# Kernel tuning notes

Measured on AMD Instinct MI355X. Metric: run time of the kernel, lower is better.

The kernel has to match this reference:

```python
import jax, jax.numpy as jnp
import numpy as np

T_MIN, T_MAX = 0.6, 1.6
SIM_LO, SIM_HI = 0.5, 0.9
LN_EPS = 1e-5


def _layernorm(x, gamma, beta):
    mu = jnp.mean(x, axis=-1, keepdims=True)
    var = jnp.mean((x - mu) ** 2, axis=-1, keepdims=True)
    return (x - mu) * jax.lax.rsqrt(var + LN_EPS) * gamma + beta


def _cos_sim(a, b, eps=1e-8):
    num = jnp.sum(a * b, axis=-1)
    na = jnp.maximum(jnp.sqrt(jnp.sum(a * a, axis=-1)), eps)
    nb = jnp.maximum(jnp.sqrt(jnp.sum(b * b, axis=-1)), eps)
    return num / (na * nb)


def setup_inputs() -> dict:
    key = jax.random.key(0)
    B, L, D = 2, 4096, 512
    ks = jax.random.split(key, 10)
    s = 0.02
    return {
        "x": jax.random.normal(ks[0], (B, L, D), dtype=jnp.float32),
        "Wq": jax.random.normal(ks[1], (D, D), dtype=jnp.float32) * s,
        "Wk": jax.random.normal(ks[2], (D, D), dtype=jnp.float32) * s,
        "Wv": jax.random.normal(ks[3], (D, D), dtype=jnp.float32) * s,
        "Wp": jax.random.normal(ks[4], (D, D), dtype=jnp.float32) * s,
        "W1": jax.random.normal(ks[5], (4 * D, D), dtype=jnp.float32) * s,
        "b1": jnp.zeros((4 * D,), dtype=jnp.float32),
        "W2": jax.random.normal(ks[6], (D, 4 * D), dtype=jnp.float32) * s,
        "b2": jnp.zeros((D,), dtype=jnp.float32),
        "gamma": jnp.ones((D,), dtype=jnp.float32),
        "beta": jnp.zeros((D,), dtype=jnp.float32),
    }


def reference(x, Wq, Wk, Wv, Wp, W1, b1, W2, b2, gamma, beta):
    B, L, D = x.shape
    xn = _layernorm(x, gamma, beta)
    # TinyAttn with T=1.0, causal=True (torch Linear: x @ W.T)
    Q = jnp.einsum("bld,ed->ble", xn, Wq)
    K = jnp.einsum("bld,ed->ble", xn, Wk)
    V = jnp.einsum("bld,ed->ble", xn, Wv)
    scores = jnp.einsum("bld,bmd->blm", Q, K) / jnp.sqrt(jnp.asarray(D, x.dtype))
    causal = jnp.triu(jnp.ones((L, L), dtype=bool), 1)
    scores = jnp.where(causal, jnp.asarray(-1e30, x.dtype), scores)
    attn = jax.nn.softmax(scores, axis=-1)  # [B, L, L]
    out = jnp.einsum("blm,bmd->bld", attn, V)
    out = jnp.einsum("bld,ed->ble", out, Wp)
    ctx = x + out
    h = _layernorm(ctx, gamma, beta)
    h = jax.nn.gelu(jnp.einsum("bld,fd->blf", h, W1) + b1, approximate=False)
    ctx = ctx + jnp.einsum("blf,df->bld", h, W2) + b2

    # AdaptiveController on last-token attention row
    last_attn = attn[:, -1]  # [B, L]
    p = jnp.clip(last_attn, 1e-9, None)
    H = -jnp.sum(p * jnp.log(p), axis=-1)  # [B]
    Hn = (H - H.min()) / (H.max() - H.min() + 1e-9)
    Hm = jax.lax.stop_gradient(jnp.mean(Hn))  # detached in torch
    T = T_MIN + (T_MAX - T_MIN) * Hm
    sim_th = SIM_HI - (SIM_HI - SIM_LO) * Hm

    # UnconsciousStack: single forward -> stack holds only the just-pushed (K, V), detached.
    q_vec = jnp.mean(Q[:, -1], axis=0, keepdims=True)  # [1, D]
    K_rep = jax.lax.stop_gradient(jnp.mean(K, axis=1))  # [B, D]
    s = jnp.mean(_cos_sim(q_vec, K_rep))  # scalar
    hit = s >= sim_th

    K_cat = jnp.concatenate([K, jax.lax.stop_gradient(K)], axis=1)  # [B, 2L, D]
    V_cat = jnp.concatenate([V, jax.lax.stop_gradient(V)], axis=1)
    scores2 = jnp.einsum("bld,bmd->blm", Q, K_cat) / jnp.sqrt(jnp.asarray(D, x.dtype))
    attn2 = jax.nn.softmax(scores2 / T, axis=-1)  # [B, L, 2L], no causal mask
    reatt = jnp.einsum("blm,bmd->bld", attn2, V_cat)
    ctx = ctx + jnp.where(hit, reatt, jnp.zeros_like(reatt))
    return ctx
```

## Files before the change

kernel.cpp:

```cpp
#include <hip/hip_runtime.h>
#include <math.h>

#define BATCH 2
#define SEQ 4096
#define DIM 512
#define FF 2048
#define NROWS (BATCH*SEQ)
#define KT 32
#define RSQRT_D 0.044194173824159216f

typedef __attribute__((ext_vector_type(8))) short short8;
typedef __attribute__((ext_vector_type(4))) short short4v;
typedef __attribute__((ext_vector_type(4))) float f32x4;

__device__ __forceinline__ float gelu_f(float v) {
    return 0.5f * v * (1.0f + erff(v * 0.70710678118654752440f));
}
__device__ __forceinline__ short bf16b(float x) {
    union { float f; unsigned u; } c; c.f = x;
    unsigned r = (c.u + 0x7FFFu + ((c.u >> 16) & 1u)) >> 16;
    return (short)r;
}
__device__ __forceinline__ float bf16f(short h) {
    union { unsigned u; float f; } c; c.u = ((unsigned)(unsigned short)h) << 16;
    return c.f;
}
__device__ __forceinline__ void gload16(const void* g, void* l) {
    __builtin_amdgcn_global_load_lds(
        (const __attribute__((address_space(1))) unsigned int*)g,
        (__attribute__((address_space(3))) unsigned int*)l, 16, 0, 0);
}
__device__ __forceinline__ float blk_sum256(float v, volatile float* sm) {
    #pragma unroll
    for (int o = 32; o; o >>= 1) v += __shfl_xor(v, o);
    __syncthreads();
    if ((threadIdx.x & 63) == 0) sm[threadIdx.x >> 6] = v;
    __syncthreads();
    return sm[0] + sm[1] + sm[2] + sm[3];
}

__global__ __launch_bounds__(256) void f2bf_all(
        const float* __restrict__ Wq, const float* __restrict__ Wk,
        const float* __restrict__ Wv, const float* __restrict__ Wp,
        const float* __restrict__ W1, const float* __restrict__ W2,
        short* __restrict__ Wcat, short* __restrict__ Wpb,
        short* __restrict__ W1b, short* __restrict__ W2b)
{
    int i = blockIdx.x * 256 + threadIdx.x;
    const float* src; short* dst; int loc;
    if      (i <  32768) { src = Wq; dst = Wcat;          loc = i; }
    else if (i <  65536) { src = Wk; dst = Wcat + 262144; loc = i - 32768; }
    else if (i <  98304) { src = Wv; dst = Wcat + 524288; loc = i - 65536; }
    else if (i < 131072) { src = Wp; dst = Wpb;           loc = i - 98304; }
    else if (i < 262144) { src = W1; dst = W1b;           loc = i - 131072; }
    else                 { src = W2; dst = W2b;           loc = i - 262144; }
    const float4* p = (const float4*)(src + (size_t)loc * 8);
    float4 a = p[0], b = p[1];
    short8 r;
    r[0]=bf16b(a.x); r[1]=bf16b(a.y); r[2]=bf16b(a.z); r[3]=bf16b(a.w);
    r[4]=bf16b(b.x); r[5]=bf16b(b.y); r[6]=bf16b(b.z); r[7]=bf16b(b.w);
    *(short8*)(dst + (size_t)loc * 8) = r;
}

__global__ __launch_bounds__(256) void ln_kernel(const float* __restrict__ x,
        const float* __restrict__ g, const float* __restrict__ be,
        short* __restrict__ o)
{
    int row  = blockIdx.x * 4 + (threadIdx.x >> 6);
    int lane = threadIdx.x & 63;
    const float4* xr = (const float4*)(x + (size_t)row * DIM);
    float4 v0 = xr[lane*2], v1 = xr[lane*2+1];
    float s = v0.x+v0.y+v0.z+v0.w + v1.x+v1.y+v1.z+v1.w;
    #pragma unroll
    for (int off = 32; off; off >>= 1) s += __shfl_xor(s, off);
    float mu = s * (1.0f/DIM);
    float d[8] = {v0.x-mu, v0.y-mu, v0.z-mu, v0.w-mu, v1.x-mu, v1.y-mu, v1.z-mu, v1.w-mu};
    float q = 0.f;
    #pragma unroll
    for (int j = 0; j < 8; ++j) q += d[j]*d[j];
    #pragma unroll
    for (int off = 32; off; off >>= 1) q += __shfl_xor(q, off);
    float rs = rsqrtf(q * (1.0f/DIM) + 1e-5f);
    const float4* g4 = (const float4*)g;
    const float4* b4 = (const float4*)be;
    float4 ga = g4[lane*2], gb = g4[lane*2+1];
    float4 ba = b4[lane*2], bb = b4[lane*2+1];
    float gv[8] = {ga.x,ga.y,ga.z,ga.w, gb.x,gb.y,gb.z,gb.w};
    float bv[8] = {ba.x,ba.y,ba.z,ba.w, bb.x,bb.y,bb.z,bb.w};
    short8 r;
    #pragma unroll
    for (int j = 0; j < 8; ++j) r[j] = bf16b(d[j]*rs*gv[j] + bv[j]);
    *(short8*)(o + (size_t)row * DIM + lane*8) = r;
}

template<int TM, int TAG>
__global__ __launch_bounds__(256) void gemm_v3(
        const short* __restrict__ A, const short* __restrict__ W,
        const float* __restrict__ bias, const float* __restrict__ res,
        float* __restrict__ Cf, short* __restrict__ Cb,
        short* __restrict__ CbK, short* __restrict__ CbV,
        int K, int sa, int sw, int sc, int act, int accum)
{
    constexpr int MI = TM / 32;
    __shared__ short As[2][TM*32];
    __shared__ short Ws[2][4096];
    int tid = threadIdx.x;
    int m0 = blockIdx.y * TM, n0 = blockIdx.x * 128;
    int w = tid >> 6, lane = tid & 63;
    int wr = (w >> 1) * (TM/2), wc = (w & 1) * 64;
    int lr = lane & 15, lg = lane >> 4;
    int srow = tid >> 2, skoff = (tid & 3) * 8;
    const short* Ab = A + (size_t)(m0 + srow) * sa + skoff;
    const short* Wb = W + (size_t)(n0 + srow) * sw + skoff;

    #define STAGE_G(buf, kk) do { \
        gload16(Ab + (kk),                    As[buf] + tid*8); \
        if constexpr (TM == 128) \
            gload16(Ab + (size_t)64*sa + (kk), As[buf] + 2048 + tid*8); \
        gload16(Wb + (kk),                    Ws[buf] + tid*8); \
        gload16(Wb + (size_t)64*sw + (kk),    Ws[buf] + 2048 + tid*8); } while(0)

    f32x4 acc[MI][4];
    f32x4 zero = {0.f, 0.f, 0.f, 0.f};
    #pragma unroll
    for (int i = 0; i < MI; ++i)
        #pragma unroll
        for (int j = 0; j < 4; ++j) acc[i][j] = zero;

    STAGE_G(0, 0);
    __syncthreads();
    int cur = 0;
    for (int k0 = 0; k0 < K; k0 += 32) {
        if (k0 + 32 < K) STAGE_G(cur ^ 1, k0 + 32);
        short8 a[MI], b[4];
        #pragma unroll
        for (int i = 0; i < MI; ++i) a[i] = *(const short8*)(As[cur] + (wr + i*16 + lr)*32 + lg*8);
        #pragma unroll
        for (int j = 0; j < 4; ++j) b[j] = *(const short8*)(Ws[cur] + (wc + j*16 + lr)*32 + lg*8);
        #pragma unroll
        for (int i = 0; i < MI; ++i)
            #pragma unroll
            for (int j = 0; j < 4; ++j)
                acc[i][j] = __builtin_amdgcn_mfma_f32_16x16x32_bf16(a[i], b[j], acc[i][j], 0, 0, 0);
        __syncthreads();
        cur ^= 1;
    }
    #undef STAGE_G

    #pragma unroll
    for (int i = 0; i < MI; ++i) {
        #pragma unroll
        for (int r = 0; r < 4; ++r) {
            size_t m = (size_t)m0 + wr + i*16 + lg*4 + r;
            #pragma unroll
            for (int j = 0; j < 4; ++j) {
                int n = n0 + wc + j*16 + lr;
                float v = acc[i][j][r];
                if (bias) v += bias[n];
                if (act)  v = gelu_f(v);
                if (CbK) {
                    int seg = n >> 9, nl = n & 511;
                    short* dst = (seg == 0) ? Cb : (seg == 1) ? CbK : CbV;
                    dst[m * 512 + nl] = bf16b(v);
                } else {
                    if (res) v += res[m * sc + n];
                    size_t idx = m * sc + n;
                    if (Cf) { if (accum) Cf[idx] += v; else Cf[idx] = v; }
                    if (Cb) Cb[idx] = bf16b(v);
                }
            }
        }
    }
}

__global__ __launch_bounds__(256) void vtrans(const short* __restrict__ V,
                                              short* __restrict__ Vt)
{
    __shared__ short t_s[64][72];
    int l0 = blockIdx.x * 64, d0 = blockIdx.y * 64, b = blockIdx.z;
    int t = threadIdx.x;
    const short* src = V + (size_t)b * SEQ * DIM;
    #pragma unroll
    for (int it = 0; it < 2; ++it) {
        int r = (t >> 3) + it * 32, c = (t & 7) * 8;
        *(short8*)&t_s[r][c] = *(const short8*)(src + (size_t)(l0 + r) * DIM + d0 + c);
    }
    __syncthreads();
    short* dst = Vt + (size_t)b * DIM * SEQ;
    #pragma unroll
    for (int it = 0; it < 2; ++it) {
        int r = (t >> 3) + it * 32, c = (t & 7) * 8;
        short8 v;
        #pragma unroll
        for (int j = 0; j < 8; ++j) v[j] = t_s[c + j][r];
        *(short8*)(dst + (size_t)(d0 + r) * SEQ + l0 + c) = v;
    }
}

__global__ __launch_bounds__(512, 2) void attn_v8(
        const short* __restrict__ Q, const short* __restrict__ K,
        const short* __restrict__ Vt, short* __restrict__ Opart,
        float* __restrict__ Mpart, float* __restrict__ Lpart,
        float scale, const float* __restrict__ scale_ptr,
        const float* __restrict__ gate, int causal, int NC, int ncs)
{
    if (gate && gate[0] == 0.0f) return;
    if (scale_ptr) scale = scale_ptr[0];
    extern __shared__ short lds[];
    short* k_s  = lds;
    short* v_s  = lds + 32768;
    short* p_s  = lds + 65536;
    float* ss_s = (float*)(lds + 69632);

    int tid = threadIdx.x, w = tid >> 6, lane = tid & 63;
    int rg = w >> 1, dh = w & 1;
    int lr = lane & 15, lg = lane >> 4;

    int bid = blockIdx.x;
    int c  = bid & (NC - 1);
    int b  = (bid >> ncs) & 1;
    int ip = bid >> (ncs + 1);
    int jj0 = ip, jj1 = 63 - ip;
    int TA = causal ? 2*(ip+1)  : 128;
    int TB = causal ? 2*(64-ip) : 128;
    int Ttot = TA + TB;
    int s0 = (Ttot * c) >> ncs, s1 = (Ttot * (c+1)) >> ncs;

    size_t bofs = (size_t)b * SEQ * DIM;
    size_t vofs = (size_t)b * DIM * SEQ;
    f32x4 zero = {0.f, 0.f, 0.f, 0.f};

    for (int sg = 0; sg < 2; ++sg) {
        int j  = sg ? jj1 : jj0;
        int ta = sg ? (max(s0, TA) - TA) : s0;
        int tb = sg ? (s1 - TA)          : min(s1, TA);
        if (ta >= tb) continue;
        int qw0 = j*64 + rg*16;

        short8 qf[8];
        #pragma unroll
        for (int kc = 0; kc < 8; ++kc)
            qf[kc] = *(const short8*)(Q + bofs + (size_t)(qw0 + lr)*DIM
                                      + dh*256 + kc*32 + lg*8);

        f32x4 o[16];
        #pragma unroll
        for (int df = 0; df < 16; ++df) o[df] = zero;
        float mreg[4] = {-1e30f,-1e30f,-1e30f,-1e30f};
        float lreg[4] = {0.f,0.f,0.f,0.f};
        int rowg[4];
        #pragma unroll
        for (int r = 0; r < 4; ++r) rowg[r] = qw0 + lg*4 + r;

        int cur = 0;
        {
            int k0s = ta * KT;
            #pragma unroll
            for (int s4 = 0; s4 < 4; ++s4) {
                int slot = tid + s4*512;
                int row = slot >> 6, cg = slot & 63;
                gload16(K + bofs + (size_t)(k0s + row)*DIM + ((cg ^ (row & 7)) << 3),
                        k_s + slot*8);
                int dpair = slot >> 3, low = slot & 7;
                int d = dpair*2 + (low & 1);
                int kg = (low >> 1) ^ (dpair & 3);
                gload16(Vt + vofs + (size_t)d*SEQ + k0s + kg*8,
                        v_s + slot*8);
            }
        }
        __syncthreads();

        for (int t = ta; t < tb; ++t) {
            int k0 = t * KT;
            if (t + 1 < tb) {
                int k0s = (t + 1) * KT;
                int bo = (cur ^ 1) * 16384;
                #pragma unroll
                for (int s4 = 0; s4 < 4; ++s4) {
                    int slot = tid + s4*512;
                    int row = slot >> 6, cg = slot & 63;
                    gload16(K + bofs + (size_t)(k0s + row)*DIM + ((cg ^ (row & 7)) << 3),
                            k_s + bo + slot*8);
                    int dpair = slot >> 3, low = slot & 7;
                    int d = dpair*2 + (low & 1);
                    int kg = (low >> 1) ^ (dpair & 3);
                    gload16(Vt + vofs + (size_t)d*SEQ + k0s + kg*8,
                            v_s + bo + slot*8);
                }
            }
            f32x4 ss[2];
            ss[0] = zero; ss[1] = zero;
            const short* kb = k_s + cur*16384;
            #pragma unroll
            for (int kc = 0; kc < 8; ++kc) {
                #pragma unroll
                for (int kf = 0; kf < 2; ++kf) {
                    int row = kf*16 + lr;
                    int dg = dh*32 + kc*4 + lg;
                    short8 kk = *(const short8*)(kb + row*512 + ((dg ^ (row & 7)) << 3));
                    ss[kf] = __builtin_amdgcn_mfma_f32_16x16x32_bf16(qf[kc], kk, ss[kf], 0, 0, 0);
                }
            }
            *(f32x4*)(ss_s + w*512 + lane*8)     = ss[0];
            *(f32x4*)(ss_s + w*512 + lane*8 + 4) = ss[1];
            asm volatile("s_waitcnt lgkmcnt(0)" ::: "memory");
            __builtin_amdgcn_s_barrier();
            __builtin_amdgcn_sched_barrier(0);
            f32x4 po0 = *(const f32x4*)(ss_s + (w^1)*512 + lane*8);
            f32x4 po1 = *(const f32x4*)(ss_s + (w^1)*512 + lane*8 + 4);
            bool needmask = causal && (k0 + KT - 1 > qw0);
            #pragma unroll
            for (int r = 0; r < 4; ++r) {
                float s0v = (ss[0][r] + po0[r]) * scale;
                float s1v = (ss[1][r] + po1[r]) * scale;
                if (needmask) {
                    if (k0 + lr      > rowg[r]) s0v = -1e30f;
                    if (k0 + 16 + lr > rowg[r]) s1v = -1e30f;
                }
                ss[0][r] = s0v; ss[1][r] = s1v;
            }
            float pm[4];
            bool tg = false;
            #pragma unroll
            for (int r = 0; r < 4; ++r) {
                pm[r] = fmaxf(ss[0][r], ss[1][r]);
                tg |= (pm[r] > mreg[r] + 8.0f);
            }
            if (__any(tg)) {
                #pragma unroll
                for (int r = 0; r < 4; ++r) {
                    float v = pm[r];
                    v = fmaxf(v, __shfl_xor(v, 1));
                    v = fmaxf(v, __shfl_xor(v, 2));
                    v = fmaxf(v, __shfl_xor(v, 4));
                    v = fmaxf(v, __shfl_xor(v, 8));
                    float nm = fmaxf(mreg[r], v);
                    float fr = __expf(mreg[r] - nm);
                    mreg[r] = nm;
                    lreg[r] *= fr;
                    #pragma unroll
                    for (int df = 0; df < 16; ++df) o[df][r] *= fr;
                }
            }
            #pragma unroll
            for (int kf = 0; kf < 2; ++kf) {
                #pragma unroll
                for (int r = 0; r < 4; ++r) {
                    float sv = ss[kf][r];
                    float p = (sv < -1e29f) ? 0.0f : __expf(sv - mreg[r]);
                    lreg[r] += p;
                    int row = lg*4 + r;
                    int oct = kf*2 + (lr >> 3);
                    p_s[w*512 + row*32 + ((oct ^ r ^ (lg & 3)) << 3) + (lr & 7)] = bf16b(p);
                }
            }
            short8 pa = *(const short8*)(p_s + w*512 + lr*32
                         + ((lg ^ (lr & 3) ^ ((lr >> 2) & 3)) << 3));
            const short* vb = v_s + cur*16384;
            #pragma unroll
            for (int df = 0; df < 16; ++df) {
                int d = dh*256 + df*16 + lr;
                int slot16 = (d >> 1)*8 + (((lg ^ ((d >> 1) & 3)) << 1) | (d & 1));
                short8 vv = *(const short8*)(vb + slot16*8);
                o[df] = __builtin_amdgcn_mfma_f32_16x16x32_bf16(pa, vv, o[df], 0, 0, 0);
            }
            __syncthreads();
            cur ^= 1;
        }

        #pragma unroll
        for (int r = 0; r < 4; ++r) {
            float v = lreg[r];
            v += __shfl_xor(v, 1);
            v += __shfl_xor(v, 2);
            v += __shfl_xor(v, 4);
            v += __shfl_xor(v, 8);
            lreg[r] = v;
        }
        int slot = (b*64 + j)*NC + c;
        size_t obase = ((size_t)slot*8 + w) * 4096;
        #pragma unroll
        for (int df = 0; df < 16; ++df) {
            short4v pk;
            #pragma unroll
            for (int r = 0; r < 4; ++r) pk[r] = bf16b(o[df][r]);
            *(short4v*)(Opart + obase + df*256 + lane*4) = pk;
        }
        if (dh == 0 && lr == 0) {
            #pragma unroll
            for (int r = 0; r < 4; ++r) {
                Mpart[slot*64 + rg*16 + lg*4 + r] = mreg[r];
                Lpart[slot*64 + rg*16 + lg*4 + r] = lreg[r];
            }
        }
    }
}

__global__ __launch_bounds__(256) void attn_merge(
        const short* __restrict__ Opart, const float* __restrict__ Mpart,
        const float* __restrict__ Lpart, short* __restrict__ attb,
        float* __restrict__ outf, const float* __restrict__ gate,
        int causal, int NC, int ncs)
{
    if (gate && gate[0] == 0.0f) return;
    __shared__ float wts[8][64];
    int j = blockIdx.x, dh = blockIdx.y, b = blockIdx.z;
    int tid = threadIdx.x;
    int ip = (j < 32) ? j : 63 - j;
    int TA = causal ? 2*(ip+1)  : 128;
    int TB = causal ? 2*(64-ip) : 128;
    int Ttot = TA + TB;
    int jstart = (j < 32) ? 0 : TA;
    int jend   = (j < 32) ? TA : Ttot;
    bool val[8];
    for (int c = 0; c < 8; ++c) {
        int sc = (Ttot * c) >> ncs, ec = (Ttot * (c+1)) >> ncs;
        val[c] = (c < NC) && (sc < jend) && (ec > jstart);
    }
    if (tid < 64) {
        float M = -1e30f;
        for (int c = 0; c < NC; ++c)
            if (val[c]) M = fmaxf(M, Mpart[((b*64 + j)*NC + c)*64 + tid]);
        float L = 0.f;
        for (int c = 0; c < NC; ++c)
            if (val[c]) L += Lpart[((b*64 + j)*NC + c)*64 + tid]
                           * __expf(Mpart[((b*64 + j)*NC + c)*64 + tid] - M);
        float invL = 1.0f / L;
        for (int c = 0; c < NC; ++c)
            wts[c][tid] = val[c]
                ? __expf(Mpart[((b*64 + j)*NC + c)*64 + tid] - M) * invL : 0.0f;
    }
    __syncthreads();
    int wv = tid >> 6, lane = tid & 63, lg = lane >> 4, lr = lane & 15;
    int region = wv*2 + dh;
    for (int df = 0; df < 16; ++df) {
        float acc[4] = {0.f, 0.f, 0.f, 0.f};
        for (int c = 0; c < NC; ++c) {
            if (!val[c]) continue;
            size_t idx = ((size_t)((b*64 + j)*NC + c)*8 + region)*4096 + df*256 + lane*4;
            short4v v = *(const short4v*)(Opart + idx);
            #pragma unroll
            for (int r = 0; r < 4; ++r)
                acc[r] += wts[c][wv*16 + lg*4 + r] * bf16f(v[r]);
        }
        #pragma unroll
        for (int r = 0; r < 4; ++r) {
            int row = j*64 + wv*16 + lg*4 + r;
            int d = dh*256 + df*16 + lr;
            size_t oidx = (size_t)b*SEQ*DIM + (size_t)row*DIM + d;
            if (attb) attb[oidx] = bf16b(acc[r]);
            else      outf[oidx] += acc[r];
        }
    }
}

__global__ __launch_bounds__(256) void lastrow_scores(const short* __restrict__ Q,
        const short* __restrict__ K, float* __restrict__ slast)
{
    __shared__ float q_l[DIM];
    int b = blockIdx.y;
    int m = blockIdx.x * 256 + threadIdx.x;
    for (int i = threadIdx.x; i < DIM; i += 256)
        q_l[i] = bf16f(Q[((size_t)b*SEQ + SEQ-1)*DIM + i]);
    __syncthreads();
    const short* kr = K + ((size_t)b*SEQ + m) * DIM;
    float s = 0.f;
    for (int d = 0; d < DIM; d += 8) {
        short8 k8 = *(const short8*)(kr + d);
        #pragma unroll
        for (int j = 0; j < 8; ++j) s += q_l[d + j] * bf16f(k8[j]);
    }
    slast[(size_t)b*SEQ + m] = s * RSQRT_D;
}

__global__ __launch_bounds__(256) void entropy_kernel(const float* __restrict__ slast,
        float* __restrict__ H)
{
    __shared__ float sm[4];
    int b = blockIdx.x, t = threadIdx.x;
    const float* s = slast + (size_t)b * SEQ;
    float v[16];
    float mx = -1e30f;
    #pragma unroll
    for (int j = 0; j < 16; ++j) { v[j] = s[t + j*256]; mx = fmaxf(mx, v[j]); }
    #pragma unroll
    for (int o = 32; o; o >>= 1) mx = fmaxf(mx, __shfl_xor(mx, o));
    __syncthreads();
    if ((t & 63) == 0) sm[t >> 6] = mx;
    __syncthreads();
    mx = fmaxf(fmaxf(sm[0], sm[1]), fmaxf(sm[2], sm[3]));
    float se = 0.f;
    #pragma unroll
    for (int j = 0; j < 16; ++j) { v[j] = expf(v[j] - mx); se += v[j]; }
    se = blk_sum256(se, sm);
    float inv = 1.0f / se;
    float h = 0.f;
    #pragma unroll
    for (int j = 0; j < 16; ++j) {
        float p = fmaxf(v[j] * inv, 1e-9f);
        h -= p * logf(p);
    }
    h = blk_sum256(h, sm);
    if (t == 0) H[b] = h;
}

__global__ __launch_bounds__(256) void krep_partial(const short* __restrict__ K,
        float* __restrict__ part)
{
    int b = blockIdx.y, j = blockIdx.x, t = threadIdx.x;
    size_t base = ((size_t)b*SEQ + (size_t)j*64) * DIM;
    float s0 = 0.f, s1 = 0.f;
    for (int r = 0; r < 64; ++r) {
        s0 += bf16f(K[base + (size_t)r*DIM + t]);
        s1 += bf16f(K[base + (size_t)r*DIM + t + 256]);
    }
    size_t o = (size_t)(b*64 + j) * DIM;
    part[o + t] = s0; part[o + t + 256] = s1;
}

__global__ __launch_bounds__(256) void scalar_kernel(const short* __restrict__ Qb,
        const float* __restrict__ part, const float* __restrict__ Hent,
        float* __restrict__ gsc)
{
    __shared__ float sm[4];
    __shared__ float sims[BATCH];
    int t = threadIdx.x;
    float qv0 = 0.5f*(bf16f(Qb[((size_t)0*SEQ + SEQ-1)*DIM + t])     + bf16f(Qb[((size_t)1*SEQ + SEQ-1)*DIM + t]));
    float qv1 = 0.5f*(bf16f(Qb[((size_t)0*SEQ + SEQ-1)*DIM + t+256]) + bf16f(Qb[((size_t)1*SEQ + SEQ-1)*DIM + t+256]));
    for (int b = 0; b < BATCH; ++b) {
        float k0 = 0.f, k1 = 0.f;
        for (int j = 0; j < 64; ++j) {
            k0 += part[(size_t)(b*64+j)*DIM + t];
            k1 += part[(size_t)(b*64+j)*DIM + t + 256];
        }
        k0 *= (1.0f/SEQ); k1 *= (1.0f/SEQ);
        float num = blk_sum256(qv0*k0 + qv1*k1, sm);
        float qq  = blk_sum256(qv0*qv0 + qv1*qv1, sm);
        float kk  = blk_sum256(k0*k0 + k1*k1, sm);
        if (t == 0) {
            float na = fmaxf(sqrtf(qq), 1e-8f);
            float nb = fmaxf(sqrtf(kk), 1e-8f);
            sims[b] = num / (na * nb);
        }
        __syncthreads();
    }
    if (t == 0) {
        float H0 = Hent[0], H1 = Hent[1];
        float mn = fminf(H0, H1), mx = fmaxf(H0, H1);
        float den = (mx - mn) + 1e-9f;
        float Hm = 0.5f*((H0 - mn)/den + (H1 - mn)/den);
        float T  = 0.6f + (1.6f - 0.6f) * Hm;
        float th = 0.9f - (0.9f - 0.5f) * Hm;
        float s  = 0.5f * (sims[0] + sims[1]);
        gsc[0] = (s >= th) ? 1.0f : 0.0f;
        gsc[1] = 1.0f / (sqrtf((float)DIM) * T);
    }
}

extern "C" void kernel_launch(void* const* d_in, const int* in_sizes, int n_in,
                              void* d_out, int out_size, void* d_ws, size_t ws_size,
                              hipStream_t stream)
{
    (void)in_sizes; (void)n_in; (void)out_size;
    const float* x     = (const float*)d_in[0];
    const float* Wq    = (const float*)d_in[1];
    const float* Wk    = (const float*)d_in[2];
    const float* Wv    = (const float*)d_in[3];
    const float* Wp    = (const float*)d_in[4];
    const float* W1    = (const float*)d_in[5];
    const float* b1    = (const float*)d_in[6];
    const float* W2    = (const float*)d_in[7];
    const float* b2    = (const float*)d_in[8];
    const float* gamma = (const float*)d_in[9];
    const float* beta  = (const float*)d_in[10];
    float* out = (float*)d_out;

    const size_t NT = (size_t)NROWS * DIM;
    short* bws   = (short*)d_ws;
    short* Qbf   = bws;
    short* Kbf   = Qbf + NT;
    short* Vt    = Kbf + NT;
    short* att   = Vt + NT;
    short* Wcat  = att + NT;
    short* Wpb   = Wcat + 786432;
    short* W1b   = Wpb + 262144;
    short* W2b   = W1b + 1048576;
    float* slast = (float*)(W2b + 1048576);
    float* Hent  = slast + 8192;
    float* kpart = Hent + 8;
    float* gsc   = kpart + 65536;

    const int NC = 4, ncs = 2;
    size_t mlsz = (size_t)128 * NC * 64;
    float* Mpart = gsc + 8;
    float* Lpart = Mpart + mlsz;
    short* xn_bf = (short*)(Lpart + mlsz);
    short* h1    = xn_bf + NT;
    short* Opart = xn_bf;

    size_t ffn_full_end = ((size_t)(h1 - bws) + (size_t)NROWS * FF) * 2;
    int ffn_full = (ws_size >= ffn_full_end + 1024);

    const int ATTN_LDS = 155648;
    hipFuncSetAttribute((const void*)attn_v8,
                        hipFuncAttributeMaxDynamicSharedMemorySize, ATTN_LDS);

    f2bf_all<<<1536, 256, 0, stream>>>(Wq, Wk, Wv, Wp, W1, W2, Wcat, Wpb, W1b, W2b);

    ln_kernel<<<NROWS/4, 256, 0, stream>>>(x, gamma, beta, xn_bf);

    gemm_v3<128,0><<<dim3(1536/128, NROWS/128), 256, 0, stream>>>(
        xn_bf, Wcat, nullptr, nullptr, nullptr, Qbf, Kbf, att,
        DIM, DIM, DIM, DIM, 0, 0);
    vtrans<<<dim3(SEQ/64, DIM/64, BATCH), 256, 0, stream>>>(att, Vt);

    attn_v8<<<64*NC, 512, ATTN_LDS, stream>>>(Qbf, Kbf, Vt, Opart, Mpart, Lpart,
                                              RSQRT_D, nullptr, nullptr, 1, NC, ncs);
    attn_merge<<<dim3(64, 2, BATCH), 256, 0, stream>>>(Opart, Mpart, Lpart, att, nullptr,
                                                       nullptr, 1, NC, ncs);

    lastrow_scores<<<dim3(SEQ/256, BATCH), 256, 0, stream>>>(Qbf, Kbf, slast);
    entropy_kernel<<<BATCH, 256, 0, stream>>>(slast, Hent);

    gemm_v3<64,1><<<dim3(DIM/128, NROWS/64), 256, 0, stream>>>(
        att, Wpb, nullptr, x, out, nullptr, nullptr, nullptr,
        DIM, DIM, DIM, DIM, 0, 0);

    ln_kernel<<<NROWS/4, 256, 0, stream>>>(out, gamma, beta, xn_bf);

    if (ffn_full) {
        gemm_v3<128,2><<<dim3(FF/128, NROWS/128), 256, 0, stream>>>(
            xn_bf, W1b, b1, nullptr, nullptr, h1, nullptr, nullptr,
            DIM, DIM, DIM, FF, 1, 0);
        gemm_v3<64,3><<<dim3(DIM/128, NROWS/64), 256, 0, stream>>>(
            h1, W2b, b2, nullptr, out, nullptr, nullptr, nullptr,
            FF, FF, FF, DIM, 0, 1);
    } else {
        for (int c = 0; c < 2; ++c) {
            gemm_v3<128,2><<<dim3(1024/128, NROWS/128), 256, 0, stream>>>(
                xn_bf, W1b + (size_t)c*1024*DIM, b1 + c*1024, nullptr,
                nullptr, h1, nullptr, nullptr,
                DIM, DIM, DIM, 1024, 1, 0);
            gemm_v3<64,3><<<dim3(DIM/128, NROWS/64), 256, 0, stream>>>(
                h1, W2b + (size_t)c*1024, (c == 0) ? b2 : nullptr, nullptr,
                out, nullptr, nullptr, nullptr,
                1024, 1024, FF, DIM, 0, 1);
        }
    }

    krep_partial<<<dim3(64, BATCH), 256, 0, stream>>>(Kbf, kpart);
    scalar_kernel<<<1, 256, 0, stream>>>(Qbf, kpart, Hent, gsc);

    attn_v8<<<64*NC, 512, ATTN_LDS, stream>>>(Qbf, Kbf, Vt, Opart, Mpart, Lpart,
                                              0.0f, gsc + 1, gsc, 0, NC, ncs);
    attn_merge<<<dim3(64, 2, BATCH), 256, 0, stream>>>(Opart, Mpart, Lpart, nullptr, out,
                                                       gsc, 0, NC, ncs);
}
```

Measured before the change: 340.8 us.

## Triple-buffer GEMM LDS staging with explicit vmcnt waits and split barriers

Converts the bf16 MFMA GEMM from double to triple buffering in shared memory. Global-to-LDS loads run two K-tiles ahead, and the code waits with explicit s_waitcnt vmcnt counts and raw s_barrier instead of __syncthreads. The aim is to hide global load latency better across K iterations. In exchange it uses more LDS per block, which may lower occupancy, and relies on hand-counted outstanding loads being correct.

```diff
diff --git a/kernel.cpp b/kernel.cpp
--- a/kernel.cpp
+++ b/kernel.cpp
@@ -94,7 +94,7 @@
 }
 
 template<int TM, int TAG>
-__global__ __launch_bounds__(256) void gemm_v3(
+__global__ __launch_bounds__(256) void gemm_v4(
         const short* __restrict__ A, const short* __restrict__ W,
         const float* __restrict__ bias, const float* __restrict__ res,
         float* __restrict__ Cf, short* __restrict__ Cb,
@@ -102,8 +102,9 @@
         int K, int sa, int sw, int sc, int act, int accum)
 {
     constexpr int MI = TM / 32;
-    __shared__ short As[2][TM*32];
-    __shared__ short Ws[2][4096];
+    constexpr int ASZ = TM * 32;
+    __shared__ short As[3 * ASZ];
+    __shared__ short Ws[3 * 4096];
     int tid = threadIdx.x;
     int m0 = blockIdx.y * TM, n0 = blockIdx.x * 128;
     int w = tid >> 6, lane = tid & 63;
@@ -114,11 +115,11 @@
     const short* Wb = W + (size_t)(n0 + srow) * sw + skoff;
 
     #define STAGE_G(buf, kk) do { \
-        gload16(Ab + (kk),                    As[buf] + tid*8); \
+        gload16(Ab + (kk),                    As + (buf)*ASZ + tid*8); \
         if constexpr (TM == 128) \
-            gload16(Ab + (size_t)64*sa + (kk), As[buf] + 2048 + tid*8); \
-        gload16(Wb + (kk),                    Ws[buf] + tid*8); \
-        gload16(Wb + (size_t)64*sw + (kk),    Ws[buf] + 2048 + tid*8); } while(0)
+            gload16(Ab + (size_t)64*sa + (kk), As + (buf)*ASZ + 2048 + tid*8); \
+        gload16(Wb + (kk),                    Ws + (buf)*4096 + tid*8); \
+        gload16(Wb + (size_t)64*sw + (kk),    Ws + (buf)*4096 + 2048 + tid*8); } while(0)
 
     f32x4 acc[MI][4];
     f32x4 zero = {0.f, 0.f, 0.f, 0.f};
@@ -127,23 +128,37 @@
         #pragma unroll
         for (int j = 0; j < 4; ++j) acc[i][j] = zero;
 
+    int NKB = K >> 5;
     STAGE_G(0, 0);
-    __syncthreads();
+    STAGE_G(1, 32);
     int cur = 0;
-    for (int k0 = 0; k0 < K; k0 += 32) {
-        if (k0 + 32 < K) STAGE_G(cur ^ 1, k0 + 32);
+    for (int kb = 0; kb < NKB; ++kb) {
+        __builtin_amdgcn_s_barrier();
+        asm volatile("" ::: "memory");
+        if (kb + 2 < NKB) {
+            int nb = cur + 2; if (nb >= 3) nb -= 3;
+            STAGE_G(nb, (kb + 2) * 32);
+            if constexpr (TM == 128) asm volatile("s_waitcnt vmcnt(8)" ::: "memory");
+            else                     asm volatile("s_waitcnt vmcnt(6)" ::: "memory");
+        } else if (kb + 1 < NKB) {
+            if constexpr (TM == 128) asm volatile("s_waitcnt vmcnt(4)" ::: "memory");
+            else                     asm volatile("s_waitcnt vmcnt(3)" ::: "memory");
+        } else {
+            asm volatile("s_waitcnt vmcnt(0)" ::: "memory");
+        }
+        __builtin_amdgcn_s_barrier();
+        asm volatile("" ::: "memory");
         short8 a[MI], b[4];
         #pragma unroll
-        for (int i = 0; i < MI; ++i) a[i] = *(const short8*)(As[cur] + (wr + i*16 + lr)*32 + lg*8);
-        #pragma unroll
-        for (int j = 0; j < 4; ++j) b[j] = *(const short8*)(Ws[cur] + (wc + j*16 + lr)*32 + lg*8);
+        for (int i = 0; i < MI; ++i) a[i] = *(const short8*)(As + cur*ASZ + (wr + i*16 + lr)*32 + lg*8);
+        #pragma unroll
+        for (int j = 0; j < 4; ++j) b[j] = *(const short8*)(Ws + cur*4096 + (wc + j*16 + lr)*32 + lg*8);
         #pragma unroll
         for (int i = 0; i < MI; ++i)
             #pragma unroll
             for (int j = 0; j < 4; ++j)
                 acc[i][j] = __builtin_amdgcn_mfma_f32_16x16x32_bf16(a[i], b[j], acc[i][j], 0, 0, 0);
-        __syncthreads();
-        cur ^= 1;
+        cur = (cur + 1 == 3) ? 0 : cur + 1;
     }
     #undef STAGE_G
 
@@ -609,7 +624,7 @@
 
     ln_kernel<<<NROWS/4, 256, 0, stream>>>(x, gamma, beta, xn_bf);
 
-    gemm_v3<128,0><<<dim3(1536/128, NROWS/128), 256, 0, stream>>>(
+    gemm_v4<128,0><<<dim3(1536/128, NROWS/128), 256, 0, stream>>>(
         xn_bf, Wcat, nullptr, nullptr, nullptr, Qbf, Kbf, att,
         DIM, DIM, DIM, DIM, 0, 0);
     vtrans<<<dim3(SEQ/64, DIM/64, BATCH), 256, 0, stream>>>(att, Vt);
@@ -622,26 +637,26 @@
     lastrow_scores<<<dim3(SEQ/256, BATCH), 256, 0, stream>>>(Qbf, Kbf, slast);
     entropy_kernel<<<BATCH, 256, 0, stream>>>(slast, Hent);
 
-    gemm_v3<64,1><<<dim3(DIM/128, NROWS/64), 256, 0, stream>>>(
+    gemm_v4<64,1><<<dim3(DIM/128, NROWS/64), 256, 0, stream>>>(
         att, Wpb, nullptr, x, out, nullptr, nullptr, nullptr,
         DIM, DIM, DIM, DIM, 0, 0);
 
     ln_kernel<<<NROWS/4, 256, 0, stream>>>(out, gamma, beta, xn_bf);
 
     if (ffn_full) {
-        gemm_v3<128,2><<<dim3(FF/128, NROWS/128), 256, 0, stream>>>(
+        gemm_v4<128,2><<<dim3(FF/128, NROWS/128), 256, 0, stream>>>(
             xn_bf, W1b, b1, nullptr, nullptr, h1, nullptr, nullptr,
             DIM, DIM, DIM, FF, 1, 0);
-        gemm_v3<64,3><<<dim3(DIM/128, NROWS/64), 256, 0, stream>>>(
+        gemm_v4<64,3><<<dim3(DIM/128, NROWS/64), 256, 0, stream>>>(
             h1, W2b, b2, nullptr, out, nullptr, nullptr, nullptr,
             FF, FF, FF, DIM, 0, 1);
     } else {
         for (int c = 0; c < 2; ++c) {
-            gemm_v3<128,2><<<dim3(1024/128, NROWS/128), 256, 0, stream>>>(
+            gemm_v4<128,2><<<dim3(1024/128, NROWS/128), 256, 0, stream>>>(
                 xn_bf, W1b + (size_t)c*1024*DIM, b1 + c*1024, nullptr,
                 nullptr, h1, nullptr, nullptr,
                 DIM, DIM, DIM, 1024, 1, 0);
-            gemm_v3<64,3><<<dim3(DIM/128, NROWS/64), 256, 0, stream>>>(
+            gemm_v4<64,3><<<dim3(DIM/128, NROWS/64), 256, 0, stream>>>(
                 h1, W2b + (size_t)c*1024, (c == 0) ? b2 : nullptr, nullptr,
                 out, nullptr, nullptr, nullptr,
                 1024, 1024, FF, DIM, 0, 1);
```

Result: no change. 337.3 us (-1.0%).

## Replace LDS-staged GEMM with direct global-to-register double-buffered MFMA loads

Applied to the files above, without the earlier changes.

The GEMM kernel no longer stages A and W tiles through shared memory with block-wide barriers. Each wave now loads its MFMA operand fragments straight from global memory into registers, using two register sets for software double buffering. This removes the LDS traffic and the __syncthreads per K step. In exchange, operands that were shared across waves through LDS are now fetched redundantly from global or L2, and each fragment load is a strided 16-byte read per lane, so coalescing is worse.

```diff
diff --git a/kernel.cpp b/kernel.cpp
--- a/kernel.cpp
+++ b/kernel.cpp
@@ -94,7 +94,7 @@
 }
 
 template<int TM, int TAG>
-__global__ __launch_bounds__(256) void gemm_v3(
+__global__ __launch_bounds__(256) void gemm_v5(
         const short* __restrict__ A, const short* __restrict__ W,
         const float* __restrict__ bias, const float* __restrict__ res,
         float* __restrict__ Cf, short* __restrict__ Cb,
@@ -102,23 +102,20 @@
         int K, int sa, int sw, int sc, int act, int accum)
 {
     constexpr int MI = TM / 32;
-    __shared__ short As[2][TM*32];
-    __shared__ short Ws[2][4096];
     int tid = threadIdx.x;
     int m0 = blockIdx.y * TM, n0 = blockIdx.x * 128;
     int w = tid >> 6, lane = tid & 63;
     int wr = (w >> 1) * (TM/2), wc = (w & 1) * 64;
     int lr = lane & 15, lg = lane >> 4;
-    int srow = tid >> 2, skoff = (tid & 3) * 8;
-    const short* Ab = A + (size_t)(m0 + srow) * sa + skoff;
-    const short* Wb = W + (size_t)(n0 + srow) * sw + skoff;
-
-    #define STAGE_G(buf, kk) do { \
-        gload16(Ab + (kk),                    As[buf] + tid*8); \
-        if constexpr (TM == 128) \
-            gload16(Ab + (size_t)64*sa + (kk), As[buf] + 2048 + tid*8); \
-        gload16(Wb + (kk),                    Ws[buf] + tid*8); \
-        gload16(Wb + (size_t)64*sw + (kk),    Ws[buf] + 2048 + tid*8); } while(0)
+
+    const short* Ap[MI];
+    #pragma unroll
+    for (int i = 0; i < MI; ++i)
+        Ap[i] = A + (size_t)(m0 + wr + i*16 + lr) * sa + lg*8;
+    const short* Bp[4];
+    #pragma unroll
+    for (int j = 0; j < 4; ++j)
+        Bp[j] = W + (size_t)(n0 + wc + j*16 + lr) * sw + lg*8;
 
     f32x4 acc[MI][4];
     f32x4 zero = {0.f, 0.f, 0.f, 0.f};
@@ -127,25 +124,32 @@
         #pragma unroll
         for (int j = 0; j < 4; ++j) acc[i][j] = zero;
 
-    STAGE_G(0, 0);
-    __syncthreads();
-    int cur = 0;
-    for (int k0 = 0; k0 < K; k0 += 32) {
-        if (k0 + 32 < K) STAGE_G(cur ^ 1, k0 + 32);
-        short8 a[MI], b[4];
-        #pragma unroll
-        for (int i = 0; i < MI; ++i) a[i] = *(const short8*)(As[cur] + (wr + i*16 + lr)*32 + lg*8);
-        #pragma unroll
-        for (int j = 0; j < 4; ++j) b[j] = *(const short8*)(Ws[cur] + (wc + j*16 + lr)*32 + lg*8);
-        #pragma unroll
-        for (int i = 0; i < MI; ++i)
-            #pragma unroll
-            for (int j = 0; j < 4; ++j)
-                acc[i][j] = __builtin_amdgcn_mfma_f32_16x16x32_bf16(a[i], b[j], acc[i][j], 0, 0, 0);
-        __syncthreads();
-        cur ^= 1;
-    }
-    #undef STAGE_G
+    short8 ax[MI], bx[4], ay[MI], by[4];
+    #define LOADS(as, bs, kk) do { \
+        _Pragma("unroll") \
+        for (int i = 0; i < MI; ++i) as[i] = *(const short8*)(Ap[i] + (kk)); \
+        _Pragma("unroll") \
+        for (int j = 0; j < 4; ++j)  bs[j] = *(const short8*)(Bp[j] + (kk)); } while(0)
+    #define COMP(as, bs) do { \
+        _Pragma("unroll") \
+        for (int i = 0; i < MI; ++i) \
+            _Pragma("unroll") \
+            for (int j = 0; j < 4; ++j) \
+                acc[i][j] = __builtin_amdgcn_mfma_f32_16x16x32_bf16(as[i], bs[j], acc[i][j], 0, 0, 0); } while(0)
+
+    LOADS(ax, bx, 0);
+    LOADS(ay, by, 32);
+    int k0 = 0;
+    for (; k0 + 64 < K; k0 += 64) {
+        COMP(ax, bx);
+        LOADS(ax, bx, k0 + 64);
+        COMP(ay, by);
+        LOADS(ay, by, k0 + 96);
+    }
+    COMP(ax, bx);
+    COMP(ay, by);
+    #undef LOADS
+    #undef COMP
 
     #pragma unroll
     for (int i = 0; i < MI; ++i) {
@@ -602,14 +606,14 @@
     int ffn_full = (ws_size >= ffn_full_end + 1024);
 
     const int ATTN_LDS = 155648;
-    hipFuncSetAttribute((const void*)attn_v8,
+    (void)hipFuncSetAttribute((const void*)attn_v8,
                         hipFuncAttributeMaxDynamicSharedMemorySize, ATTN_LDS);
 
     f2bf_all<<<1536, 256, 0, stream>>>(Wq, Wk, Wv, Wp, W1, W2, Wcat, Wpb, W1b, W2b);
 
     ln_kernel<<<NROWS/4, 256, 0, stream>>>(x, gamma, beta, xn_bf);
 
-    gemm_v3<128,0><<<dim3(1536/128, NROWS/128), 256, 0, stream>>>(
+    gemm_v5<128,0><<<dim3(1536/128, NROWS/128), 256, 0, stream>>>(
         xn_bf, Wcat, nullptr, nullptr, nullptr, Qbf, Kbf, att,
         DIM, DIM, DIM, DIM, 0, 0);
     vtrans<<<dim3(SEQ/64, DIM/64, BATCH), 256, 0, stream>>>(att, Vt);
@@ -622,26 +626,26 @@
     lastrow_scores<<<dim3(SEQ/256, BATCH), 256, 0, stream>>>(Qbf, Kbf, slast);
     entropy_kernel<<<BATCH, 256, 0, stream>>>(slast, Hent);
 
-    gemm_v3<64,1><<<dim3(DIM/128, NROWS/64), 256, 0, stream>>>(
+    gemm_v5<64,1><<<dim3(DIM/128, NROWS/64), 256, 0, stream>>>(
         att, Wpb, nullptr, x, out, nullptr, nullptr, nullptr,
         DIM, DIM, DIM, DIM, 0, 0);
 
     ln_kernel<<<NROWS/4, 256, 0, stream>>>(out, gamma, beta, xn_bf);
 
     if (ffn_full) {
-        gemm_v3<128,2><<<dim3(FF/128, NROWS/128), 256, 0, stream>>>(
+        gemm_v5<128,2><<<dim3(FF/128, NROWS/128), 256, 0, stream>>>(
             xn_bf, W1b, b1, nullptr, nullptr, h1, nullptr, nullptr,
             DIM, DIM, DIM, FF, 1, 0);
-        gemm_v3<64,3><<<dim3(DIM/128, NROWS/64), 256, 0, stream>>>(
+        gemm_v5<64,3><<<dim3(DIM/128, NROWS/64), 256, 0, stream>>>(
             h1, W2b, b2, nullptr, out, nullptr, nullptr, nullptr,
             FF, FF, FF, DIM, 0, 1);
     } else {
         for (int c = 0; c < 2; ++c) {
-            gemm_v3<128,2><<<dim3(1024/128, NROWS/128), 256, 0, stream>>>(
+            gemm_v5<128,2><<<dim3(1024/128, NROWS/128), 256, 0, stream>>>(
                 xn_bf, W1b + (size_t)c*1024*DIM, b1 + c*1024, nullptr,
                 nullptr, h1, nullptr, nullptr,
                 DIM, DIM, DIM, 1024, 1, 0);
-            gemm_v3<64,3><<<dim3(DIM/128, NROWS/64), 256, 0, stream>>>(
+            gemm_v5<64,3><<<dim3(DIM/128, NROWS/64), 256, 0, stream>>>(
                 h1, W2b + (size_t)c*1024, (c == 0) ? b2 : nullptr, nullptr,
                 out, nullptr, nullptr, nullptr,
                 1024, 1024, FF, DIM, 0, 1);
```

After: 449.8 us. 32.0% more time.
